# Performance work log

Measured on AMD Instinct MI355X. Metric: run time of the kernel, lower is better.

Reference implementation:

```python
import jax, jax.numpy as jnp
import numpy as np

W = 64          # word_embedding_size
ES = 64         # entity_embedding_size
H = 4           # head_num
DH = W // H
K = 3           # convolution_num
NW, NQ, NE, NR = 50000, 20000, 200000, 100000
LQ, LR, EP, B = 8, 16, 500000, 1024
D = ES + W      # propagated entity feature dim


def _mhsa_mean(x, Wq, bq, Wk, bk, Wv, bv, Wo, bo):
    # x: [N, L, W] -> [N, W]; standard multi-head self-attention then mean over L
    N, L, _ = x.shape
    q = (x @ Wq + bq).reshape(N, L, H, DH)
    k = (x @ Wk + bk).reshape(N, L, H, DH)
    v = (x @ Wv + bv).reshape(N, L, H, DH)
    s = jnp.einsum('nlhd,nmhd->nhlm', q, k) / jnp.sqrt(jnp.asarray(DH, x.dtype))
    a = jax.nn.softmax(s, axis=-1)
    o = jnp.einsum('nhlm,nmhd->nlhd', a, v).reshape(N, L, W)
    return (o @ Wo + bo).mean(axis=1)


def setup_inputs() -> dict:
    key = jax.random.key(0)
    ks = jax.random.split(key, 20)
    f = jnp.float32
    inp = {
        'word_emb': jax.random.normal(ks[0], (NW, W), f) * 0.02,
        'entity_emb': jax.random.normal(ks[1], (NE, ES), f) * 0.02,
        'Wq': jax.random.normal(ks[2], (W, W), f) * (1.0 / np.sqrt(W)),
        'bq': jnp.zeros((W,), f),
        'Wk': jax.random.normal(ks[3], (W, W), f) * (1.0 / np.sqrt(W)),
        'bk': jnp.zeros((W,), f),
        'Wv': jax.random.normal(ks[4], (W, W), f) * (1.0 / np.sqrt(W)),
        'bv': jnp.zeros((W,), f),
        'Wo': jax.random.normal(ks[5], (W, W), f) * (1.0 / np.sqrt(W)),
        'bo': jnp.zeros((W,), f),
        'review_words': jax.random.randint(ks[6], (NR, LR), 0, NW),
        'query_words_graph': jax.random.randint(ks[7], (NQ, LQ), 0, NW),
        'profile_dst': jax.random.randint(ks[8], (NR,), 0, NE),
        'pur_src': jax.random.randint(ks[9], (EP,), 0, NE),
        'pur_dst': jax.random.randint(ks[10], (EP,), 0, NE),
        'pur_qid': jax.random.randint(ks[11], (EP,), 0, NQ),
        'users': jax.random.randint(ks[12], (B,), 0, NE),
        'items': jax.random.randint(ks[13], (B,), 0, NE),
        'negs': jax.random.randint(ks[14], (B,), 0, NE),
        'query_words': jax.random.randint(ks[15], (B, LQ), 0, NW),
    }
    return inp


def reference(word_emb, entity_emb, Wq, bq, Wk, bk, Wv, bv, Wo, bo,
              review_words, query_words_graph, profile_dst,
              pur_src, pur_dst, pur_qid, users, items, negs, query_words):
    seg = jax.ops.segment_sum
    attn = lambda x: _mhsa_mean(x, Wq, bq, Wk, bk, Wv, bv, Wo, bo)
    we = word_emb.at[0].set(0.0)  # padding_idx=0

    # composes: word -> review / query (mailbox attention reduce)
    rev_h = attn(we[review_words])              # [NR, W]
    q_h = attn(we[query_words_graph])           # [NQ, W]
    q_e0 = jnp.concatenate([jnp.zeros((NQ, ES), we.dtype), q_h], axis=-1)  # [NQ, D]

    # profiles: review -> entity, mean by in-degree
    deg_p = jnp.clip(seg(jnp.ones((NR,), we.dtype), profile_dst, num_segments=NE), 1.0)[:, None]
    prof = seg(rev_h, profile_dst, num_segments=NE) / deg_p   # [NE, W]
    e = jnp.concatenate([entity_emb, prof], axis=-1)          # e_0: [NE, D]

    # deg_i = out_deg(purchased) + out_deg(purchased_by), clamped
    ones_e = jnp.ones((EP,), we.dtype)
    deg_i = jnp.clip(seg(ones_e, pur_src, num_segments=NE)
                     + seg(ones_e, pur_dst, num_segments=NE), 1.0)[:, None]
    inv = 1.0 / jnp.sqrt(deg_i)                               # [NE, 1]

    es = [e]
    for _ in range(K):
        msg = e * inv                                         # e_k / sqrt(deg_i)
        m_pur = e[pur_src] + q_e0[pur_qid] * inv[pur_src]     # msg_u_i UDF
        nxt = seg(m_pur, pur_dst, num_segments=NE) \
            + seg(msg[pur_dst], pur_src, num_segments=NE)     # purchased_by (reverse)
        e = nxt * inv
        es.append(e)
    efin = sum(es) / (K + 1)                                  # [NE, D]

    # batch scoring
    u = efin[users]
    qb = attn(we[query_words])                                # [B, W]
    p = u + jnp.concatenate([jnp.zeros((B, ES), we.dtype), qb], axis=-1)
    pos = jnp.sum(p * efin[items], axis=-1)
    neg = jnp.sum(p * efin[negs], axis=-1)
    loss = -jnp.mean(jax.nn.log_sigmoid(pos - neg))           # BPR loss
    return loss
```

## Files before the change

kernel.cpp:

```cpp
#include <hip/hip_runtime.h>
#include <hip/hip_fp8.h>
#include <cstdint>

#define CDIV(a,b) (((a)+(b)-1)/(b))

typedef __attribute__((ext_vector_type(8))) short bf16x8;
typedef __attribute__((ext_vector_type(4))) float f32x4;
typedef __attribute__((ext_vector_type(8))) float f32x8;
typedef __attribute__((ext_vector_type(4))) _Float16 half4;
typedef __attribute__((ext_vector_type(8))) _Float16 half8;

#define QK_SCALE 32.0f
#define SCORE_SCALE (0.25f / (QK_SCALE * QK_SCALE))
#define EXP2_C (SCORE_SCALE * 1.44269504089f)

#define ES_SCALE 64.0f

__device__ __forceinline__ float bf2f(short s) {
    return __builtin_bit_cast(float, ((unsigned)(unsigned short)s) << 16);
}
__device__ __forceinline__ short rtne(float f) {
    const unsigned u = __builtin_bit_cast(unsigned, f);
    return (short)((u + 0x7fffu + ((u >> 16) & 1u)) >> 16);
}
__device__ __forceinline__ unsigned pack2r(float lo, float hi) {
    return (unsigned)(unsigned short)rtne(lo) | ((unsigned)(unsigned short)rtne(hi) << 16);
}
__device__ __forceinline__ float fp8tof(unsigned char b) {
    __hip_fp8_e4m3 t; t.__x = b; return (float)t;
}
__device__ __forceinline__ unsigned char ftofp8(float f) {
    __hip_fp8_e4m3 t(f); return t.__x;
}
__device__ __forceinline__ f32x8 fp8x8tof32(long v) {
    union { long l; unsigned char b[8]; } u; u.l = v;
    f32x8 r;
    #pragma unroll
    for (int j = 0; j < 8; ++j) r[j] = fp8tof(u.b[j]);
    return r;
}
__device__ __forceinline__ long f32x8tofp8(f32x8 a) {
    union { long l; unsigned char b[8]; } u;
    #pragma unroll
    for (int j = 0; j < 8; ++j) u.b[j] = ftofp8(a[j]);
    return u.l;
}

template<int CTRL>
__device__ __forceinline__ float dpp_add(float x) {
    const int t = __builtin_amdgcn_update_dpp(0, __builtin_bit_cast(int, x),
                                              CTRL, 0xf, 0xf, true);
    return x + __builtin_bit_cast(float, t);
}
__device__ __forceinline__ float rowsum16(float x) {
    x = dpp_add<0x108>(x);
    x = dpp_add<0x104>(x);
    x = dpp_add<0x102>(x);
    x = dpp_add<0x101>(x);
    return x;
}


__device__ __forceinline__ void prep_body(int bid,
    const float* __restrict__ we, const short* __restrict__ Wt,
    const float* __restrict__ bq, const float* __restrict__ bk,
    const float* __restrict__ bv, unsigned char* __restrict__ WQKV, int NW)
{
    const int wave = threadIdx.x >> 6;
    const int lane = threadIdx.x & 63;
    const int quad = lane >> 4;
    const int lm   = lane & 15;
    const int ntiles = CDIV(NW, 16);

    bf16x8 bfr[3][4][2];
    #pragma unroll
    for (int p = 0; p < 3; ++p)
        #pragma unroll
        for (int nt = 0; nt < 4; ++nt)
            #pragma unroll
            for (int kh = 0; kh < 2; ++kh)
                bfr[p][nt][kh] = *(const bf16x8*)(Wt + ((p*64 + nt*16 + lm)*64) + kh*32 + quad*8);
    float bias[3][4];
    #pragma unroll
    for (int nt = 0; nt < 4; ++nt) {
        bias[0][nt] = bq[nt*16 + lm];
        bias[1][nt] = bk[nt*16 + lm];
        bias[2][nt] = bv[nt*16 + lm];
    }

    #pragma unroll
    for (int t = 0; t < 4; ++t) {
        const int tile = (bid*4 + wave)*4 + t;
        if (tile >= ntiles) return;
        const int wb = tile*16;
        int w = wb + lm;
        if (w >= NW) w = NW - 1;
        const float* xr = we + (size_t)w*64;
        union { unsigned u[4]; bf16x8 v; } a0, a1;
        const float4 f0 = *(const float4*)(xr + quad*8);
        const float4 f1 = *(const float4*)(xr + quad*8 + 4);
        const float4 f2 = *(const float4*)(xr + 32 + quad*8);
        const float4 f3 = *(const float4*)(xr + 32 + quad*8 + 4);
        a0.u[0] = pack2r(f0.x, f0.y); a0.u[1] = pack2r(f0.z, f0.w);
        a0.u[2] = pack2r(f1.x, f1.y); a0.u[3] = pack2r(f1.z, f1.w);
        a1.u[0] = pack2r(f2.x, f2.y); a1.u[1] = pack2r(f2.z, f2.w);
        a1.u[2] = pack2r(f3.x, f3.y); a1.u[3] = pack2r(f3.z, f3.w);
        if (w == 0) {
            a0.u[0]=0u; a0.u[1]=0u; a0.u[2]=0u; a0.u[3]=0u;
            a1.u[0]=0u; a1.u[1]=0u; a1.u[2]=0u; a1.u[3]=0u;
        }
        #pragma unroll
        for (int p = 0; p < 3; ++p) {
            #pragma unroll
            for (int nt = 0; nt < 4; ++nt) {
                f32x4 c = {bias[p][nt], bias[p][nt], bias[p][nt], bias[p][nt]};
                c = __builtin_amdgcn_mfma_f32_16x16x32_bf16(a0.v, bfr[p][nt][0], c, 0, 0, 0);
                c = __builtin_amdgcn_mfma_f32_16x16x32_bf16(a1.v, bfr[p][nt][1], c, 0, 0, 0);
                #pragma unroll
                for (int r = 0; r < 4; ++r) {
                    const int w2 = wb + quad*4 + r;
                    if (w2 < NW) {
                        unsigned char* rowo = WQKV + (size_t)w2*192;
                        const int base = (p == 2) ? 128 : (p == 0) ? 64 : 0;
                        rowo[base + nt*16 + lm] = ftofp8(c[r] * QK_SCALE);
                    }
                }
            }
        }
    }
}

__device__ __forceinline__ void fill_body(int bid,
    const int* __restrict__ src, const int* __restrict__ dst,
    const int* __restrict__ qid,
    int* __restrict__ curC, int2* __restrict__ cmb2, int EP)
{
    const int t = bid*256 + threadIdx.x;
    if (t >= EP) return;
    const int s = src[t], d = dst[t];
    const int p1 = atomicAdd(&curC[d], 1);
    int2 e1; e1.x = s; e1.y = qid[t];
    cmb2[p1] = e1;
    const int p2 = atomicAdd(&curC[s], 1);
    int2 e2; e2.x = d | (int)0x80000000; e2.y = 0;
    cmb2[p2] = e2;
}

__device__ __forceinline__ void expand_body(int bid, int nb, unsigned targ,
    const int* __restrict__ slist, const int* __restrict__ pn,
    const int* __restrict__ offC, const int* __restrict__ endC,
    const int2* __restrict__ cmb2, unsigned* __restrict__ lev,
    int* __restrict__ dl1, int* __restrict__ dn1,
    int* __restrict__ dl2, int* __restrict__ dn2)
{
    const int n = *pn;
    const int stride = nb * 256;
    for (int t = bid*256 + threadIdx.x; t < n; t += stride) {
        const int v = slist[t];
        const int b0 = offC[v], e0 = endC[v];
        for (int i = b0; i < e0; ++i) {
            const int u = cmb2[i].x & 0x7fffffff;
            const unsigned old = atomicMax(&lev[u], targ);
            if (old < targ) {
                dl1[atomicAdd(dn1, 1)] = u;
                if (dl2) dl2[atomicAdd(dn2, 1)] = u;
            }
        }
    }
}

__device__ __forceinline__ void finalize_body(int bid,
    const float* __restrict__ emb, const float* __restrict__ prof,
    unsigned char* __restrict__ e8, float* __restrict__ inv,
    const unsigned* __restrict__ deg_p, const unsigned* __restrict__ cntC, int NE)
{
    const int t = bid*256 + threadIdx.x;
    const int v = t >> 5;
    if (v >= NE) return;
    const int c = (t & 31) * 4;
    float4 ev;
    if (c < 64) {
        ev = *(const float4*)&emb[(size_t)v*64 + c];
    } else {
        ev = *(const float4*)&prof[(size_t)v*64 + (c - 64)];
        const unsigned dp = deg_p[v];
        const float r = 1.0f / (float)(dp > 1u ? dp : 1u);
        ev.x *= r; ev.y *= r; ev.z *= r; ev.w *= r;
    }
    union { unsigned u; unsigned char b[4]; } pk;
    pk.b[0] = ftofp8(ev.x * ES_SCALE);
    pk.b[1] = ftofp8(ev.y * ES_SCALE);
    pk.b[2] = ftofp8(ev.z * ES_SCALE);
    pk.b[3] = ftofp8(ev.w * ES_SCALE);
    *(unsigned*)&e8[(size_t)v*128 + c] = pk.u;
    if (c == 0) {
        const unsigned di = cntC[v];
        inv[v] = 1.0f / sqrtf((float)(di > 1u ? di : 1u));
    }
}

__device__ __forceinline__ void gather_body(int bid,
    const unsigned char* __restrict__ e8, const int* __restrict__ users,
    const int* __restrict__ items, const int* __restrict__ negs,
    float* __restrict__ acc, int B)
{
    const int t = bid*256 + threadIdx.x;
    const int r = t >> 4;
    if (r >= 3*B) return;
    const int c = (t & 15) * 8;
    const int which = r / B, b = r - which*B;
    const int idx = (which == 0) ? users[b] : (which == 1) ? items[b] : negs[b];
    const long ev = *(const long*)&e8[(size_t)idx*128 + c];
    f32x8 a = *(const f32x8*)&acc[(size_t)r*128 + c];
    a += fp8x8tof32(ev);
    *(f32x8*)&acc[(size_t)r*128 + c] = a;
}

__device__ __forceinline__ void prop1_body(int bid, int nb,
    const unsigned char* __restrict__ e_cur, const _Float16* __restrict__ q_h16,
    const float* __restrict__ inv,
    const int* __restrict__ offC, const int* __restrict__ endC,
    const int2* __restrict__ cmb2,
    const int* __restrict__ list, const int* __restrict__ pn,
    unsigned char* __restrict__ e_nxt, _Float16* __restrict__ qc)
{
    const int n = *pn;
    const int stride = nb * 256;
    for (int t = bid*256 + threadIdx.x; (t >> 4) < n; t += stride) {
        const int v = list[t >> 4];
        const int c = (t & 15) * 8;
        const bool qlane = (c >= 64);
        f32x8 a  = {0.f,0.f,0.f,0.f,0.f,0.f,0.f,0.f};
        f32x8 qa = {0.f,0.f,0.f,0.f,0.f,0.f,0.f,0.f};
        const int b0 = offC[v], e0 = endC[v];
        for (int i = b0; i < e0; ++i) {
            const int2 e = cmb2[i];
            const int u = e.x & 0x7fffffff;
            const float w = (e.x < 0) ? inv[u] : 1.0f;
            a += fp8x8tof32(*(const long*)&e_cur[(size_t)u*128 + c]) * w;
            if (e.x >= 0 && qlane) {
                const half8 qh = *(const half8*)&q_h16[(size_t)e.y*64 + (c - 64)];
                qa += __builtin_convertvector(qh, f32x8) * inv[u];
            }
        }
        if (qlane) {
            qa *= ES_SCALE;
            *(half8*)&qc[(size_t)v*64 + (c - 64)] = __builtin_convertvector(qa, half8);
            a += qa;
        }
        a *= inv[v];
        *(long*)&e_nxt[(size_t)v*128 + c] = f32x8tofp8(a);
    }
}

__device__ __forceinline__ void prop_list_body(int bid, int nb,
    const unsigned char* __restrict__ e_cur, const _Float16* __restrict__ qc,
    const float* __restrict__ inv,
    const int* __restrict__ offC, const int* __restrict__ endC,
    const int2* __restrict__ cmb2,
    const int* __restrict__ list, const int* __restrict__ pn,
    unsigned char* __restrict__ e_nxt)
{
    const int n = *pn;
    const int stride = nb * 256;
    for (int t = bid*256 + threadIdx.x; (t >> 4) < n; t += stride) {
        const int v = list[t >> 4];
        const int c = (t & 15) * 8;
        f32x8 a = {0.f,0.f,0.f,0.f,0.f,0.f,0.f,0.f};
        if (c >= 64) {
            const half8 q = *(const half8*)&qc[(size_t)v*64 + (c - 64)];
            a = __builtin_convertvector(q, f32x8);
        }
        const int b0 = offC[v], e0 = endC[v];
        int un = (b0 < e0) ? cmb2[b0].x : 0;
        for (int i = b0; i < e0; ++i) {
            const int uc = un;
            if (i + 1 < e0) un = cmb2[i + 1].x;
            const int u = uc & 0x7fffffff;
            const long es = *(const long*)&e_cur[(size_t)u*128 + c];
            const float w = (uc < 0) ? inv[u] : 1.0f;
            a += fp8x8tof32(es) * w;
        }
        a *= inv[v];
        *(long*)&e_nxt[(size_t)v*128 + c] = f32x8tofp8(a);
    }
}

struct TileRegs { int4 v0; long qf[4], kf[4]; };

__device__ __forceinline__ void load_tile(
    const unsigned char* __restrict__ WQKV, int w, int quad, TileRegs& t)
{
    const unsigned char* row = WQKV + (size_t)w * 192;
    t.v0 = *(const int4*)(row + 128 + quad*16);
    #pragma unroll
    for (int h = 0; h < 4; ++h) {
        if (quad < 2) {
            t.kf[h] = *(const long*)(row +      h*16 + quad*8);
            t.qf[h] = *(const long*)(row + 64 + h*16 + quad*8);
        } else {
            t.kf[h] = 0; t.qf[h] = 0;
        }
    }
}

template<int L, int MODE>
__device__ __forceinline__ void attn_body(
    unsigned char* __restrict__ smem,
    const unsigned char* __restrict__ WQKV, const int* __restrict__ words,
    const short* __restrict__ WoT, const float* __restrict__ bo,
    int N, void* __restrict__ outp, const int* __restrict__ sidx, int bid)
{
    constexpr int SPT = 16 / L;
    constexpr int SB  = 16 * SPT;
    unsigned char (*v_s)[16*80] = (unsigned char (*)[16*80])smem;
    float (*pbar_s)[64]         = (float (*)[64])(smem + 5120);
    float (*mo_s)[68]           = (float (*)[68])(smem + 6144);

    const int wave = threadIdx.x >> 6;
    const int lane = threadIdx.x & 63;
    const int quad = lane >> 4;
    const int lm   = lane & 15;
    const int tok_total = N * L;
    const float invL = 1.0f / ((float)L * QK_SCALE);

    int wid[4];
    #pragma unroll
    for (int t = 0; t < 4; ++t) {
        int tg = (bid*16 + wave*4 + t)*16 + lm;
        if (tg >= tok_total) tg = tok_total - 1;
        wid[t] = words[tg];
    }

    TileRegs cur, nxt;
    load_tile(WQKV, wid[0], quad, cur);

    #pragma unroll
    for (int ti = 0; ti < 4; ++ti) {
        if (ti < 3) load_tile(WQKV, wid[ti+1], quad, nxt);

        *(int4*)&v_s[wave][lm*80 + quad*16] = cur.v0;

        const bool mvalid = (SPT == 1) ? true : ((quad >> 1) == ((lm >> 3) & 1));

        #pragma unroll
        for (int h = 0; h < 4; ++h) {
            const f32x4 s4 = __builtin_amdgcn_mfma_f32_16x16x32_fp8_fp8(
                cur.kf[h], cur.qf[h], (f32x4){0.f,0.f,0.f,0.f}, 0, 0, 0);
            float sv0 = s4[0], sv1 = s4[1], sv2 = s4[2], sv3 = s4[3];
            if (!mvalid) { sv0 = sv1 = sv2 = sv3 = -3.0e38f; }
            float p0 = __builtin_amdgcn_exp2f(sv0*EXP2_C),
                  p1 = __builtin_amdgcn_exp2f(sv1*EXP2_C),
                  p2 = __builtin_amdgcn_exp2f(sv2*EXP2_C),
                  p3 = __builtin_amdgcn_exp2f(sv3*EXP2_C);
            float sm = p0+p1+p2+p3;
            sm += __shfl_xor(sm, 16, 64);
            sm += __shfl_xor(sm, 32, 64);
            const float rinv = __builtin_amdgcn_rcpf(sm);
            p0 *= rinv; p1 *= rinv; p2 *= rinv; p3 *= rinv;
            p0 = rowsum16(p0); p1 = rowsum16(p1);
            p2 = rowsum16(p2); p3 = rowsum16(p3);
            if (lm == 0) {
                pbar_s[wave][h*16 + quad*4 + 0] = p0 * invL;
                pbar_s[wave][h*16 + quad*4 + 1] = p1 * invL;
                pbar_s[wave][h*16 + quad*4 + 2] = p2 * invL;
                pbar_s[wave][h*16 + quad*4 + 3] = p3 * invL;
            }
        }

        #pragma unroll
        for (int s = 0; s < SPT; ++s) {
            f32x4 pb[4];
            #pragma unroll
            for (int j = 0; j < 4; ++j)
                pb[j] = *(const f32x4*)&pbar_s[wave][quad*16 + j*4];
            float o = 0.f;
            #pragma unroll
            for (int j2 = 0; j2 < L; ++j2) {
                const int m = s*L + j2;
                o += pb[m >> 2][m & 3] * fp8tof(v_s[wave][m*80 + lane]);
            }
            mo_s[(wave*4+ti)*SPT + s][lane] = o;
        }

        if (ti < 3) {
            cur.v0 = nxt.v0;
            #pragma unroll
            for (int h = 0; h < 4; ++h) { cur.qf[h] = nxt.qf[h]; cur.kf[h] = nxt.kf[h]; }
        }
    }
    __syncthreads();

    const int col = wave*16 + lm;
    const short* bT = WoT + col*64;
    const bf16x8 b0 = *(const bf16x8*)(bT + quad*8);
    const bf16x8 b1 = *(const bf16x8*)(bT + 32 + quad*8);
    const float boc = bo[col];
    #pragma unroll
    for (int rt = 0; rt < SPT; ++rt) {
        const float* ar = mo_s[rt*16 + lm];
        const float4 fA0 = *(const float4*)(ar + quad*8);
        const float4 fA1 = *(const float4*)(ar + quad*8 + 4);
        const float4 fA2 = *(const float4*)(ar + 32 + quad*8);
        const float4 fA3 = *(const float4*)(ar + 32 + quad*8 + 4);
        union { unsigned u[4]; bf16x8 v; } a0, a1;
        a0.u[0] = pack2r(fA0.x, fA0.y); a0.u[1] = pack2r(fA0.z, fA0.w);
        a0.u[2] = pack2r(fA1.x, fA1.y); a0.u[3] = pack2r(fA1.z, fA1.w);
        a1.u[0] = pack2r(fA2.x, fA2.y); a1.u[1] = pack2r(fA2.z, fA2.w);
        a1.u[2] = pack2r(fA3.x, fA3.y); a1.u[3] = pack2r(fA3.z, fA3.w);
        f32x4 c = {boc, boc, boc, boc};
        c = __builtin_amdgcn_mfma_f32_16x16x32_bf16(a0.v, b0, c, 0, 0, 0);
        c = __builtin_amdgcn_mfma_f32_16x16x32_bf16(a1.v, b1, c, 0, 0, 0);
        #pragma unroll
        for (int r = 0; r < 4; ++r) {
            const int seq = bid*SB + rt*16 + quad*4 + r;
            if (seq < N) {
                if (MODE == 0)
                    ((float*)outp)[(size_t)seq*64 + col] = c[r];
                else if (MODE == 1)
                    atomicAdd(&((float*)outp)[(size_t)sidx[seq]*64 + col], c[r]);
                else
                    ((_Float16*)outp)[(size_t)seq*64 + col] = (_Float16)c[r];
            }
        }
    }
}


__global__ __launch_bounds__(256) void misc_kernel(
    const int* __restrict__ src, const int* __restrict__ dst,
    unsigned* __restrict__ cntC, int EP,
    const int* __restrict__ pdst, unsigned* __restrict__ deg_p, int NR,
    const float* __restrict__ Wo, short* __restrict__ WoT,
    const float* __restrict__ Wq, const float* __restrict__ Wk,
    const float* __restrict__ Wv, short* __restrict__ Wt,
    const int* __restrict__ users, const int* __restrict__ items,
    const int* __restrict__ negs, int B, unsigned* __restrict__ lev,
    int* __restrict__ listS, int* __restrict__ list2, int* __restrict__ list1,
    int* __restrict__ nS, int* __restrict__ n2, int* __restrict__ n1,
    float4* __restrict__ prof_z, float4* __restrict__ acc_z,
    int prof4, int acc4, int nbM0)
{
    if ((int)blockIdx.x >= nbM0) {
        const int z = ((int)blockIdx.x - nbM0)*256 + (int)threadIdx.x;
        const float4 zero4 = {0.f, 0.f, 0.f, 0.f};
        if (z < prof4) prof_z[z] = zero4;
        else if (z - prof4 < acc4) acc_z[z - prof4] = zero4;
        return;
    }
    const int t = blockIdx.x*256 + threadIdx.x;
    if (t < EP) {
        const int s = src[t], d = dst[t];
        atomicAdd(&cntC[d], 1u); atomicAdd(&cntC[s], 1u);
    }
    if (t < NR) atomicAdd(&deg_p[pdst[t]], 1u);
    if (t < 4096) {
        const int j = t >> 6, k = t & 63;
        WoT[j*64 + k] = rtne(Wo[k*64 + j]);
    }
    if (t < 3*4096) {
        const int p = t >> 12, n = (t >> 6) & 63, k = t & 63;
        const float* W = (p==0) ? Wq : (p==1) ? Wk : Wv;
        Wt[t] = rtne(W[k*64 + n]);
    }
    if (t < 3*B) {
        const int which = t / B, b = t - which*B;
        const int v = (which == 0) ? users[b] : (which == 1) ? items[b] : negs[b];
        const unsigned old = atomicMax(&lev[v], 3u);
        if (old < 3u) {
            listS[atomicAdd(nS, 1)] = v;
            list2[atomicAdd(n2, 1)] = v;
            list1[atomicAdd(n1, 1)] = v;
        }
    }
}

#define SCAN_CHUNK 2048

__device__ __forceinline__ void scan_reduce_body(int b,
    const unsigned* __restrict__ cnt, unsigned* __restrict__ part, int n)
{
    const int base = b * SCAN_CHUNK;
    unsigned s = 0;
    #pragma unroll
    for (int i = 0; i < 8; ++i) {
        const int idx = base + i*256 + threadIdx.x;
        if (idx < n) s += cnt[idx];
    }
    #pragma unroll
    for (int off = 1; off < 64; off <<= 1) s += __shfl_xor(s, off, 64);
    __shared__ unsigned wsum[4];
    if ((threadIdx.x & 63) == 0) wsum[threadIdx.x >> 6] = s;
    __syncthreads();
    if (threadIdx.x == 0) part[b] = wsum[0]+wsum[1]+wsum[2]+wsum[3];
}

__global__ __launch_bounds__(256) void mega_scan_prep(
    const unsigned* __restrict__ cnt, unsigned* __restrict__ part, int n, int NB,
    const float* __restrict__ we, const short* __restrict__ Wt,
    const float* __restrict__ bq, const float* __restrict__ bk,
    const float* __restrict__ bv, unsigned char* __restrict__ WQKV, int NW)
{
    const int b = blockIdx.x;
    if (b < NB) scan_reduce_body(b, cnt, part, n);
    else        prep_body(b - NB, we, Wt, bq, bk, bv, WQKV, NW);
}

__global__ __launch_bounds__(1024) void scan_part_kernel(
    unsigned* __restrict__ part, int NB)
{
    __shared__ unsigned a[1024];
    const int t = threadIdx.x;
    a[t] = (t < NB) ? part[t] : 0u;
    __syncthreads();
    for (int d = 1; d < 1024; d <<= 1) {
        const unsigned xa = (t >= d) ? a[t-d] : 0u;
        __syncthreads();
        a[t] += xa;
        __syncthreads();
    }
    if (t < NB) part[t] = (t > 0) ? a[t-1] : 0u;
}

__global__ __launch_bounds__(256) void scan_final_kernel(
    const unsigned* __restrict__ cnt, const unsigned* __restrict__ part,
    int* __restrict__ off, int* __restrict__ cur, int n)
{
    const int b = blockIdx.x;
    __shared__ unsigned v[SCAN_CHUNK];
    __shared__ unsigned tsum[256];
    const int base = b * SCAN_CHUNK;
    const int t = threadIdx.x;
    #pragma unroll
    for (int i = 0; i < 8; ++i) {
        const int idx = base + i*256 + t;
        v[i*256 + t] = (idx < n) ? cnt[idx] : 0u;
    }
    __syncthreads();
    unsigned s = 0;
    #pragma unroll
    for (int i = 0; i < 8; ++i) s += v[t*8 + i];
    tsum[t] = s;
    __syncthreads();
    for (int d = 1; d < 256; d <<= 1) {
        const unsigned x = (t >= d) ? tsum[t-d] : 0u;
        __syncthreads();
        tsum[t] += x;
        __syncthreads();
    }
    unsigned run = ((t > 0) ? tsum[t-1] : 0u) + part[b];
    #pragma unroll
    for (int i = 0; i < 8; ++i) {
        const int idx = base + t*8 + i;
        if (idx < n) { off[idx] = (int)run; cur[idx] = (int)run; run += v[t*8+i]; }
    }
}

__global__ __launch_bounds__(256) void mega_attn(
    const unsigned char* __restrict__ WQKV,
    const int* __restrict__ src, const int* __restrict__ dst,
    const int* __restrict__ qid, int* __restrict__ curC,
    int2* __restrict__ cmb2, int EP, int nbF,
    const int* __restrict__ w1, int N1, float* __restrict__ o1,
    const int* __restrict__ sidx1, int nb1,
    const int* __restrict__ w2, int N2, _Float16* __restrict__ o2, int nb2,
    const int* __restrict__ w3, int N3, float* __restrict__ o3,
    const short* __restrict__ WoT, const float* __restrict__ bo)
{
    __shared__ __align__(16) unsigned char smem[6144 + 32*68*4];
    const int b = blockIdx.x;
    const int total = (int)gridDim.x;
    int W = (3*total)/5;
    if (W < nbF) W = nbF;
    const int wstart = total - W;
    int ba = b;
    if (b >= wstart) {
        const int local = b - wstart;
        const int f0 = (int)(((long)local * nbF) / W);
        const int f1 = (int)(((long)(local + 1) * nbF) / W);
        if (f1 > f0) {
            fill_body(f0, src, dst, qid, curC, cmb2, EP);
            return;
        }
        ba = b - f0;
    }
    if (ba < nb1)
        attn_body<16,1>(smem, WQKV, w1, WoT, bo, N1, o1, sidx1, ba);
    else if (ba < nb1 + nb2)
        attn_body<8,2>(smem, WQKV, w2, WoT, bo, N2, o2, nullptr, ba - nb1);
    else
        attn_body<8,0>(smem, WQKV, w3, WoT, bo, N3, o3, nullptr, ba - nb1 - nb2);
}

__global__ __launch_bounds__(256) void expand_kernel(
    unsigned targ, const int* __restrict__ slist, const int* __restrict__ pn,
    const int* __restrict__ offC, const int* __restrict__ endC,
    const int2* __restrict__ cmb2, unsigned* __restrict__ lev,
    int* __restrict__ dl1, int* __restrict__ dn1,
    int* __restrict__ dl2, int* __restrict__ dn2)
{
    expand_body(blockIdx.x, gridDim.x, targ, slist, pn, offC, endC, cmb2, lev,
                dl1, dn1, dl2, dn2);
}

__global__ __launch_bounds__(256) void mega_final(
    const int* __restrict__ list2, const int* __restrict__ n2,
    const int* __restrict__ offC, const int* __restrict__ endC,
    const int2* __restrict__ cmb2, unsigned* __restrict__ lev,
    int* __restrict__ list1, int* __restrict__ n1,
    const float* __restrict__ emb, const float* __restrict__ prof,
    unsigned char* __restrict__ e8, float* __restrict__ inv,
    const unsigned* __restrict__ deg_p, const unsigned* __restrict__ cntC, int NE)
{
    const int b = blockIdx.x;
    if (b < 256)
        expand_body(b, 256, 1u, list2, n2, offC, endC, cmb2, lev,
                    list1, n1, nullptr, nullptr);
    else
        finalize_body(b - 256, emb, prof, e8, inv, deg_p, cntC, NE);
}

__global__ __launch_bounds__(256) void mega_prop1(
    const unsigned char* __restrict__ e_cur, const _Float16* __restrict__ q_h16,
    const float* __restrict__ inv,
    const int* __restrict__ offC, const int* __restrict__ endC,
    const int2* __restrict__ cmb2,
    const int* __restrict__ list1, const int* __restrict__ n1,
    unsigned char* __restrict__ e_nxt, _Float16* __restrict__ qc,
    const int* __restrict__ users, const int* __restrict__ items,
    const int* __restrict__ negs, float* __restrict__ acc, int B)
{
    const int b = blockIdx.x;
    if (b < 2048) prop1_body(b, 2048, e_cur, q_h16, inv, offC, endC, cmb2,
                             list1, n1, e_nxt, qc);
    else          gather_body(b - 2048, e_cur, users, items, negs, acc, B);
}

__global__ __launch_bounds__(256) void mega_pg(
    const unsigned char* __restrict__ e_cur, const _Float16* __restrict__ qc,
    const float* __restrict__ inv,
    const int* __restrict__ offC, const int* __restrict__ endC,
    const int2* __restrict__ cmb2,
    const int* __restrict__ list2, const int* __restrict__ n2,
    unsigned char* __restrict__ e_nxt,
    const int* __restrict__ users, const int* __restrict__ items,
    const int* __restrict__ negs, float* __restrict__ acc, int B)
{
    const int b = blockIdx.x;
    if (b < 512) prop_list_body(b, 512, e_cur, qc, inv, offC, endC, cmb2,
                                list2, n2, e_nxt);
    else         gather_body(b - 512, e_cur, users, items, negs, acc, B);
}

__global__ __launch_bounds__(256) void prop_batch_kernel(
    const unsigned char* __restrict__ e_cur, const _Float16* __restrict__ qc,
    const float* __restrict__ inv,
    const int* __restrict__ offC, const int* __restrict__ endC,
    const int2* __restrict__ cmb2,
    const int* __restrict__ users, const int* __restrict__ items,
    const int* __restrict__ negs, float* __restrict__ acc, int B)
{
    const int t = blockIdx.x*256 + threadIdx.x;
    const int r = t >> 4;
    if (r >= 3*B) return;
    const int c = (t & 15) * 8;
    const int which = r / B, b = r - which*B;
    const int v = (which == 0) ? users[b] : (which == 1) ? items[b] : negs[b];
    f32x8 a = {0.f,0.f,0.f,0.f,0.f,0.f,0.f,0.f};
    if (c >= 64) {
        const half8 q = *(const half8*)&qc[(size_t)v*64 + (c - 64)];
        a = __builtin_convertvector(q, f32x8);
    }
    const int b0 = offC[v], e0 = endC[v];
    int un = (b0 < e0) ? cmb2[b0].x : 0;
    for (int i = b0; i < e0; ++i) {
        const int uc = un;
        if (i + 1 < e0) un = cmb2[i + 1].x;
        const int u = uc & 0x7fffffff;
        const long es = *(const long*)&e_cur[(size_t)u*128 + c];
        const float w = (uc < 0) ? inv[u] : 1.0f;
        a += fp8x8tof32(es) * w;
    }
    a *= inv[v];
    a += fp8x8tof32(*(const long*)&e_cur[(size_t)v*128 + c]);
    f32x8 ac = *(const f32x8*)&acc[(size_t)r*128 + c];
    ac += a;
    *(f32x8*)&acc[(size_t)r*128 + c] = ac;
}

__global__ __launch_bounds__(128) void loss_kernel(
    const float* __restrict__ acc, const float* __restrict__ qb,
    float* __restrict__ out, int B, float invB)
{
    const int b = blockIdx.x, d = threadIdx.x;
    const float u = acc[(size_t)b*128 + d] * (0.25f / ES_SCALE);
    const float p = u + (d >= 64 ? qb[(size_t)b*64 + (d - 64)] : 0.f);
    const float ei = acc[(size_t)(B + b)*128 + d];
    const float en = acc[(size_t)(2*B + b)*128 + d];
    float x = p * (ei - en) * (0.25f / ES_SCALE);
    #pragma unroll
    for (int off = 1; off < 64; off <<= 1) x += __shfl_xor(x, off, 64);
    __shared__ float wred[2];
    if ((threadIdx.x & 63) == 0) wred[threadIdx.x >> 6] = x;
    __syncthreads();
    if (threadIdx.x == 0) {
        const float xx = wred[0] + wred[1];
        const float ls = fminf(xx, 0.f) - log1pf(expf(-fabsf(xx)));
        atomicAdd(out, -ls * invB);
    }
}

extern "C" void kernel_launch(void* const* d_in, const int* in_sizes, int n_in,
                              void* d_out, int out_size, void* d_ws, size_t ws_size,
                              hipStream_t stream)
{
    const float* word_emb        = (const float*)d_in[0];
    const float* entity_emb      = (const float*)d_in[1];
    const float* Wq = (const float*)d_in[2];  const float* bq = (const float*)d_in[3];
    const float* Wk = (const float*)d_in[4];  const float* bk = (const float*)d_in[5];
    const float* Wv = (const float*)d_in[6];  const float* bv = (const float*)d_in[7];
    const float* Wo = (const float*)d_in[8];  const float* bo = (const float*)d_in[9];
    const int* review_words      = (const int*)d_in[10];
    const int* query_words_graph = (const int*)d_in[11];
    const int* profile_dst       = (const int*)d_in[12];
    const int* pur_src           = (const int*)d_in[13];
    const int* pur_dst           = (const int*)d_in[14];
    const int* pur_qid           = (const int*)d_in[15];
    const int* users             = (const int*)d_in[16];
    const int* items             = (const int*)d_in[17];
    const int* negs              = (const int*)d_in[18];
    const int* query_words       = (const int*)d_in[19];

    const int NW = in_sizes[0]  / 64;
    const int NE = in_sizes[1]  / 64;
    const int NR = in_sizes[10] / 16;
    const int NQ = in_sizes[11] / 8;
    const int EP = in_sizes[13];
    const int B  = in_sizes[16];
    const int NB = CDIV(NE, SCAN_CHUNK);

    char* ws = (char*)d_ws;
    size_t off = 0;
    auto alloc = [&](size_t bytes) -> char* {
        char* q = ws + off; off += (bytes + 255) & ~(size_t)255; return q;
    };
    float*         prof  = (float*)         alloc((size_t)NE*64*4);
    unsigned char* e8A   = (unsigned char*) alloc((size_t)NE*128);
    unsigned char* e8B   = (unsigned char*) alloc((size_t)NE*128);
    _Float16*      q_h16 = (_Float16*)      alloc((size_t)NQ*64*2);
    float*         qb    = (float*)         alloc((size_t)B*64*4);
    float*         acc   = (float*)         alloc((size_t)3*B*128*4);
    unsigned*  deg_p   = (unsigned*) alloc((size_t)NE*4);
    unsigned*  cntC    = (unsigned*) alloc((size_t)NE*4);
    unsigned*  lev     = (unsigned*) alloc((size_t)NE*4);
    int*       fcnt    = (int*)      alloc(256);
    int*       offC    = (int*)      alloc((size_t)NE*4);
    int*       curC    = (int*)      alloc((size_t)NE*4);
    int2*      cmb2    = (int2*)     alloc((size_t)2*EP*8);
    int*       listS   = (int*)      alloc((size_t)3*B*4);
    int*       list2   = (int*)      alloc((size_t)NE*4);
    int*       list1   = (int*)      alloc((size_t)NE*4);
    float*     inv     = (float*)    alloc((size_t)NE*4);
    unsigned*  part    = (unsigned*) alloc((size_t)NB*4);
    short*     WoT     = (short*)    alloc((size_t)64*64*2);
    short*     Wt      = (short*)    alloc((size_t)3*64*64*2);

    if (off > ws_size) return;

    unsigned char* WQKV = e8A;
    _Float16* qc = (_Float16*)prof;
    int* nS = fcnt; int* n2 = fcnt + 1; int* n1 = fcnt + 2;

    const size_t zlen = (size_t)((char*)fcnt - (char*)deg_p) + 256;
    hipMemsetAsync(deg_p, 0, zlen, stream);
    hipMemsetAsync(d_out, 0, (size_t)out_size*4, stream);

    const int nbM0  = CDIV(EP, 256);
    const int prof4 = NE*16;
    const int acc4  = 3*B*32;
    const int nbZ   = CDIV(prof4 + acc4, 256);
    misc_kernel<<<nbM0 + nbZ, 256, 0, stream>>>(pur_src, pur_dst, cntC, EP,
        profile_dst, deg_p, NR, Wo, WoT, Wq, Wk, Wv, Wt,
        users, items, negs, B, lev, listS, list2, list1, nS, n2, n1,
        (float4*)prof, (float4*)acc, prof4, acc4, nbM0);

    const int nbP = CDIV(CDIV(NW, 16), 16);
    mega_scan_prep<<<NB + nbP, 256, 0, stream>>>(cntC, part, NE, NB,
        word_emb, Wt, bq, bk, bv, WQKV, NW);
    scan_part_kernel<<<1, 1024, 0, stream>>>(part, NB);
    scan_final_kernel<<<NB, 256, 0, stream>>>(cntC, part, offC, curC, NE);

    const int nbF = CDIV(EP, 256);
    const int nb1 = CDIV(NR, 16), nb2 = CDIV(NQ, 32), nb3 = CDIV(B, 32);
    mega_attn<<<nb1 + nb2 + nb3 + nbF, 256, 0, stream>>>(WQKV,
        pur_src, pur_dst, pur_qid, curC, cmb2, EP, nbF,
        review_words, NR, prof, profile_dst, nb1,
        query_words_graph, NQ, q_h16, nb2,
        query_words, B, qb, WoT, bo);

    expand_kernel<<<64, 256, 0, stream>>>(2u, listS, nS, offC, curC, cmb2, lev,
        list2, n2, list1, n1);

    mega_final<<<256 + CDIV(NE*32, 256), 256, 0, stream>>>(
        list2, n2, offC, curC, cmb2, lev, list1, n1,
        entity_emb, prof, e8A, inv, deg_p, cntC, NE);

    mega_prop1<<<2048 + CDIV(3*B*16, 256), 256, 0, stream>>>(
        e8A, q_h16, inv, offC, curC, cmb2, list1, n1, e8B, qc,
        users, items, negs, acc, B);

    mega_pg<<<512 + CDIV(3*B*16, 256), 256, 0, stream>>>(
        e8B, qc, inv, offC, curC, cmb2, list2, n2, e8A,
        users, items, negs, acc, B);

    prop_batch_kernel<<<CDIV(3*B*16, 256), 256, 0, stream>>>(e8A, qc, inv,
        offC, curC, cmb2, users, items, negs, acc, B);

    loss_kernel<<<B, 128, 0, stream>>>(acc, qb, (float*)d_out, B, 1.0f / (float)B);
}
```

Measured before the change: 457.0 us.

## Replace CSR frontier expansion with edge-parallel BFS fused into earlier kernels

The frontier expansion used to walk CSR adjacency from a seed list. It now scans the raw edge list in parallel, checking both endpoints' levels. This removes the need for the CSR to exist, so level-2 expansion moves into the scan/prep kernel and level-1 expansion into the attention/fill kernel. Two standalone launches (expand_kernel and the expansion half of mega_final) go away. The cost is reading all EP edges twice instead of only the frontier's neighbours. Correctness also now depends on level-2 expansion finishing before level-1 expansion begins, which kernel ordering provides.

New measurement: 800.2 us. +75.1%, slower.

```diff
diff --git a/kernel.cpp b/kernel.cpp
--- a/kernel.cpp
+++ b/kernel.cpp
@@ -146,24 +146,28 @@
     cmb2[p2] = e2;
 }
 
-__device__ __forceinline__ void expand_body(int bid, int nb, unsigned targ,
-    const int* __restrict__ slist, const int* __restrict__ pn,
-    const int* __restrict__ offC, const int* __restrict__ endC,
-    const int2* __restrict__ cmb2, unsigned* __restrict__ lev,
+__device__ __forceinline__ void eexp_body(int bid, int nb, unsigned targ,
+    const int* __restrict__ src, const int* __restrict__ dst, int EP,
+    unsigned* __restrict__ lev,
     int* __restrict__ dl1, int* __restrict__ dn1,
     int* __restrict__ dl2, int* __restrict__ dn2)
 {
-    const int n = *pn;
     const int stride = nb * 256;
-    for (int t = bid*256 + threadIdx.x; t < n; t += stride) {
-        const int v = slist[t];
-        const int b0 = offC[v], e0 = endC[v];
-        for (int i = b0; i < e0; ++i) {
-            const int u = cmb2[i].x & 0x7fffffff;
-            const unsigned old = atomicMax(&lev[u], targ);
+    for (int t = bid*256 + threadIdx.x; t < EP; t += stride) {
+        const int s = src[t], d = dst[t];
+        const unsigned ls = lev[s], ld = lev[d];
+        if (ls > targ && ld < targ) {
+            const unsigned old = atomicMax(&lev[d], targ);
             if (old < targ) {
-                dl1[atomicAdd(dn1, 1)] = u;
-                if (dl2) dl2[atomicAdd(dn2, 1)] = u;
+                dl1[atomicAdd(dn1, 1)] = d;
+                if (dl2) dl2[atomicAdd(dn2, 1)] = d;
+            }
+        }
+        if (ld > targ && ls < targ) {
+            const unsigned old = atomicMax(&lev[s], targ);
+            if (old < targ) {
+                dl1[atomicAdd(dn1, 1)] = s;
+                if (dl2) dl2[atomicAdd(dn2, 1)] = s;
             }
         }
     }
@@ -499,11 +503,17 @@
     const unsigned* __restrict__ cnt, unsigned* __restrict__ part, int n, int NB,
     const float* __restrict__ we, const short* __restrict__ Wt,
     const float* __restrict__ bq, const float* __restrict__ bk,
-    const float* __restrict__ bv, unsigned char* __restrict__ WQKV, int NW)
+    const float* __restrict__ bv, unsigned char* __restrict__ WQKV, int NW, int nbP,
+    const int* __restrict__ src, const int* __restrict__ dst, int EP,
+    unsigned* __restrict__ lev,
+    int* __restrict__ list2, int* __restrict__ n2,
+    int* __restrict__ list1, int* __restrict__ n1)
 {
     const int b = blockIdx.x;
-    if (b < NB) scan_reduce_body(b, cnt, part, n);
-    else        prep_body(b - NB, we, Wt, bq, bk, bv, WQKV, NW);
+    if (b < NB)            scan_reduce_body(b, cnt, part, n);
+    else if (b < NB + nbP) prep_body(b - NB, we, Wt, bq, bk, bv, WQKV, NW);
+    else                   eexp_body(b - NB - nbP, 256, 2u, src, dst, EP, lev,
+                                     list2, n2, list1, n1);
 }
 
 __global__ __launch_bounds__(1024) void scan_part_kernel(
@@ -561,6 +571,7 @@
     const int* __restrict__ src, const int* __restrict__ dst,
     const int* __restrict__ qid, int* __restrict__ curC,
     int2* __restrict__ cmb2, int EP, int nbF,
+    unsigned* __restrict__ lev, int* __restrict__ list1, int* __restrict__ n1,
     const int* __restrict__ w1, int N1, float* __restrict__ o1,
     const int* __restrict__ sidx1, int nb1,
     const int* __restrict__ w2, int N2, _Float16* __restrict__ o2, int nb2,
@@ -570,16 +581,21 @@
     __shared__ __align__(16) unsigned char smem[6144 + 32*68*4];
     const int b = blockIdx.x;
     const int total = (int)gridDim.x;
+    const int nbS = nbF + 128;
     int W = (3*total)/5;
-    if (W < nbF) W = nbF;
+    if (W < nbS) W = nbS;
     const int wstart = total - W;
     int ba = b;
     if (b >= wstart) {
         const int local = b - wstart;
-        const int f0 = (int)(((long)local * nbF) / W);
-        const int f1 = (int)(((long)(local + 1) * nbF) / W);
+        const int f0 = (int)(((long)local * nbS) / W);
+        const int f1 = (int)(((long)(local + 1) * nbS) / W);
         if (f1 > f0) {
-            fill_body(f0, src, dst, qid, curC, cmb2, EP);
+            if (f0 < nbF)
+                fill_body(f0, src, dst, qid, curC, cmb2, EP);
+            else
+                eexp_body(f0 - nbF, 128, 1u, src, dst, EP, lev,
+                          list1, n1, nullptr, nullptr);
             return;
         }
         ba = b - f0;
@@ -592,32 +608,12 @@
         attn_body<8,0>(smem, WQKV, w3, WoT, bo, N3, o3, nullptr, ba - nb1 - nb2);
 }
 
-__global__ __launch_bounds__(256) void expand_kernel(
-    unsigned targ, const int* __restrict__ slist, const int* __restrict__ pn,
-    const int* __restrict__ offC, const int* __restrict__ endC,
-    const int2* __restrict__ cmb2, unsigned* __restrict__ lev,
-    int* __restrict__ dl1, int* __restrict__ dn1,
-    int* __restrict__ dl2, int* __restrict__ dn2)
-{
-    expand_body(blockIdx.x, gridDim.x, targ, slist, pn, offC, endC, cmb2, lev,
-                dl1, dn1, dl2, dn2);
-}
-
-__global__ __launch_bounds__(256) void mega_final(
-    const int* __restrict__ list2, const int* __restrict__ n2,
-    const int* __restrict__ offC, const int* __restrict__ endC,
-    const int2* __restrict__ cmb2, unsigned* __restrict__ lev,
-    int* __restrict__ list1, int* __restrict__ n1,
+__global__ __launch_bounds__(256) void finalize_kernel(
     const float* __restrict__ emb, const float* __restrict__ prof,
     unsigned char* __restrict__ e8, float* __restrict__ inv,
     const unsigned* __restrict__ deg_p, const unsigned* __restrict__ cntC, int NE)
 {
-    const int b = blockIdx.x;
-    if (b < 256)
-        expand_body(b, 256, 1u, list2, n2, offC, endC, cmb2, lev,
-                    list1, n1, nullptr, nullptr);
-    else
-        finalize_body(b - 256, emb, prof, e8, inv, deg_p, cntC, NE);
+    finalize_body(blockIdx.x, emb, prof, e8, inv, deg_p, cntC, NE);
 }
 
 __global__ __launch_bounds__(256) void mega_prop1(
@@ -785,24 +781,22 @@
         (float4*)prof, (float4*)acc, prof4, acc4, nbM0);
 
     const int nbP = CDIV(CDIV(NW, 16), 16);
-    mega_scan_prep<<<NB + nbP, 256, 0, stream>>>(cntC, part, NE, NB,
-        word_emb, Wt, bq, bk, bv, WQKV, NW);
+    mega_scan_prep<<<NB + nbP + 256, 256, 0, stream>>>(cntC, part, NE, NB,
+        word_emb, Wt, bq, bk, bv, WQKV, NW, nbP,
+        pur_src, pur_dst, EP, lev, list2, n2, list1, n1);
     scan_part_kernel<<<1, 1024, 0, stream>>>(part, NB);
     scan_final_kernel<<<NB, 256, 0, stream>>>(cntC, part, offC, curC, NE);
 
     const int nbF = CDIV(EP, 256);
     const int nb1 = CDIV(NR, 16), nb2 = CDIV(NQ, 32), nb3 = CDIV(B, 32);
-    mega_attn<<<nb1 + nb2 + nb3 + nbF, 256, 0, stream>>>(WQKV,
+    mega_attn<<<nb1 + nb2 + nb3 + nbF + 128, 256, 0, stream>>>(WQKV,
         pur_src, pur_dst, pur_qid, curC, cmb2, EP, nbF,
+        lev, list1, n1,
         review_words, NR, prof, profile_dst, nb1,
         query_words_graph, NQ, q_h16, nb2,
         query_words, B, qb, WoT, bo);
 
-    expand_kernel<<<64, 256, 0, stream>>>(2u, listS, nS, offC, curC, cmb2, lev,
-        list2, n2, list1, n1);
-
-    mega_final<<<256 + CDIV(NE*32, 256), 256, 0, stream>>>(
-        list2, n2, offC, curC, cmb2, lev, list1, n1,
+    finalize_kernel<<<CDIV(NE*32, 256), 256, 0, stream>>>(
         entity_emb, prof, e8A, inv, deg_p, cntC, NE);
 
     mega_prop1<<<2048 + CDIV(3*B*16, 256), 256, 0, stream>>>(
```

## Record per-edge ranks during counting and fold partial scan into final scan

Applied to the files above, without the earlier changes.

The degree-counting atomics now store their returned old value as a per-edge rank, so CSR fill computes slots as offset plus rank instead of doing a second round of atomics. The separate single-block partial-sum scan kernel is removed; each final-scan block sums the preceding block partials itself with wave reductions, and the end-pointer array is written directly as offset plus count. This removes one kernel launch and the fill atomics, at the cost of two extra EP-sized int arrays written and read, plus a small redundant prefix sum in every scan block.

Result: faster. 436.9 us (-4.4%).

```diff
diff --git a/kernel.cpp b/kernel.cpp
--- a/kernel.cpp
+++ b/kernel.cpp
@@ -133,15 +133,17 @@
 __device__ __forceinline__ void fill_body(int bid,
     const int* __restrict__ src, const int* __restrict__ dst,
     const int* __restrict__ qid,
-    int* __restrict__ curC, int2* __restrict__ cmb2, int EP)
+    const int* __restrict__ offC,
+    const int* __restrict__ rankD, const int* __restrict__ rankS,
+    int2* __restrict__ cmb2, int EP)
 {
     const int t = bid*256 + threadIdx.x;
     if (t >= EP) return;
     const int s = src[t], d = dst[t];
-    const int p1 = atomicAdd(&curC[d], 1);
+    const int p1 = offC[d] + rankD[t];
     int2 e1; e1.x = s; e1.y = qid[t];
     cmb2[p1] = e1;
-    const int p2 = atomicAdd(&curC[s], 1);
+    const int p2 = offC[s] + rankS[t];
     int2 e2; e2.x = d | (int)0x80000000; e2.y = 0;
     cmb2[p2] = e2;
 }
@@ -429,7 +431,8 @@
 
 __global__ __launch_bounds__(256) void misc_kernel(
     const int* __restrict__ src, const int* __restrict__ dst,
-    unsigned* __restrict__ cntC, int EP,
+    unsigned* __restrict__ cntC, int* __restrict__ rankD, int* __restrict__ rankS,
+    int EP,
     const int* __restrict__ pdst, unsigned* __restrict__ deg_p, int NR,
     const float* __restrict__ Wo, short* __restrict__ WoT,
     const float* __restrict__ Wq, const float* __restrict__ Wk,
@@ -451,7 +454,8 @@
     const int t = blockIdx.x*256 + threadIdx.x;
     if (t < EP) {
         const int s = src[t], d = dst[t];
-        atomicAdd(&cntC[d], 1u); atomicAdd(&cntC[s], 1u);
+        rankD[t] = (int)atomicAdd(&cntC[d], 1u);
+        rankS[t] = (int)atomicAdd(&cntC[s], 1u);
     }
     if (t < NR) atomicAdd(&deg_p[pdst[t]], 1u);
     if (t < 4096) {
@@ -506,22 +510,6 @@
     else        prep_body(b - NB, we, Wt, bq, bk, bv, WQKV, NW);
 }
 
-__global__ __launch_bounds__(1024) void scan_part_kernel(
-    unsigned* __restrict__ part, int NB)
-{
-    __shared__ unsigned a[1024];
-    const int t = threadIdx.x;
-    a[t] = (t < NB) ? part[t] : 0u;
-    __syncthreads();
-    for (int d = 1; d < 1024; d <<= 1) {
-        const unsigned xa = (t >= d) ? a[t-d] : 0u;
-        __syncthreads();
-        a[t] += xa;
-        __syncthreads();
-    }
-    if (t < NB) part[t] = (t > 0) ? a[t-1] : 0u;
-}
-
 __global__ __launch_bounds__(256) void scan_final_kernel(
     const unsigned* __restrict__ cnt, const unsigned* __restrict__ part,
     int* __restrict__ off, int* __restrict__ cur, int n)
@@ -529,14 +517,20 @@
     const int b = blockIdx.x;
     __shared__ unsigned v[SCAN_CHUNK];
     __shared__ unsigned tsum[256];
+    __shared__ unsigned wsum2[4];
     const int base = b * SCAN_CHUNK;
     const int t = threadIdx.x;
+    unsigned pv = (t < b) ? part[t] : 0u;
+    #pragma unroll
+    for (int o = 1; o < 64; o <<= 1) pv += __shfl_xor(pv, o, 64);
+    if ((t & 63) == 0) wsum2[t >> 6] = pv;
     #pragma unroll
     for (int i = 0; i < 8; ++i) {
         const int idx = base + i*256 + t;
         v[i*256 + t] = (idx < n) ? cnt[idx] : 0u;
     }
     __syncthreads();
+    const unsigned pbase = wsum2[0]+wsum2[1]+wsum2[2]+wsum2[3];
     unsigned s = 0;
     #pragma unroll
     for (int i = 0; i < 8; ++i) s += v[t*8 + i];
@@ -548,18 +542,24 @@
         tsum[t] += x;
         __syncthreads();
     }
-    unsigned run = ((t > 0) ? tsum[t-1] : 0u) + part[b];
+    unsigned run = ((t > 0) ? tsum[t-1] : 0u) + pbase;
     #pragma unroll
     for (int i = 0; i < 8; ++i) {
         const int idx = base + t*8 + i;
-        if (idx < n) { off[idx] = (int)run; cur[idx] = (int)run; run += v[t*8+i]; }
+        if (idx < n) {
+            const unsigned c = v[t*8+i];
+            off[idx] = (int)run;
+            cur[idx] = (int)(run + c);
+            run += c;
+        }
     }
 }
 
 __global__ __launch_bounds__(256) void mega_attn(
     const unsigned char* __restrict__ WQKV,
     const int* __restrict__ src, const int* __restrict__ dst,
-    const int* __restrict__ qid, int* __restrict__ curC,
+    const int* __restrict__ qid, const int* __restrict__ offC,
+    const int* __restrict__ rankD, const int* __restrict__ rankS,
     int2* __restrict__ cmb2, int EP, int nbF,
     const int* __restrict__ w1, int N1, float* __restrict__ o1,
     const int* __restrict__ sidx1, int nb1,
@@ -579,7 +579,7 @@
         const int f0 = (int)(((long)local * nbF) / W);
         const int f1 = (int)(((long)(local + 1) * nbF) / W);
         if (f1 > f0) {
-            fill_body(f0, src, dst, qid, curC, cmb2, EP);
+            fill_body(f0, src, dst, qid, offC, rankD, rankS, cmb2, EP);
             return;
         }
         ba = b - f0;
@@ -757,6 +757,8 @@
     int*       offC    = (int*)      alloc((size_t)NE*4);
     int*       curC    = (int*)      alloc((size_t)NE*4);
     int2*      cmb2    = (int2*)     alloc((size_t)2*EP*8);
+    int*       rankD   = (int*)      alloc((size_t)EP*4);
+    int*       rankS   = (int*)      alloc((size_t)EP*4);
     int*       listS   = (int*)      alloc((size_t)3*B*4);
     int*       list2   = (int*)      alloc((size_t)NE*4);
     int*       list1   = (int*)      alloc((size_t)NE*4);
@@ -779,7 +781,8 @@
     const int prof4 = NE*16;
     const int acc4  = 3*B*32;
     const int nbZ   = CDIV(prof4 + acc4, 256);
-    misc_kernel<<<nbM0 + nbZ, 256, 0, stream>>>(pur_src, pur_dst, cntC, EP,
+    misc_kernel<<<nbM0 + nbZ, 256, 0, stream>>>(pur_src, pur_dst, cntC,
+        rankD, rankS, EP,
         profile_dst, deg_p, NR, Wo, WoT, Wq, Wk, Wv, Wt,
         users, items, negs, B, lev, listS, list2, list1, nS, n2, n1,
         (float4*)prof, (float4*)acc, prof4, acc4, nbM0);
@@ -787,13 +790,12 @@
     const int nbP = CDIV(CDIV(NW, 16), 16);
     mega_scan_prep<<<NB + nbP, 256, 0, stream>>>(cntC, part, NE, NB,
         word_emb, Wt, bq, bk, bv, WQKV, NW);
-    scan_part_kernel<<<1, 1024, 0, stream>>>(part, NB);
     scan_final_kernel<<<NB, 256, 0, stream>>>(cntC, part, offC, curC, NE);
 
     const int nbF = CDIV(EP, 256);
     const int nb1 = CDIV(NR, 16), nb2 = CDIV(NQ, 32), nb3 = CDIV(B, 32);
     mega_attn<<<nb1 + nb2 + nb3 + nbF, 256, 0, stream>>>(WQKV,
-        pur_src, pur_dst, pur_qid, curC, cmb2, EP, nbF,
+        pur_src, pur_dst, pur_qid, offC, rankD, rankS, cmb2, EP, nbF,
         review_words, NR, prof, profile_dst, nb1,
         query_words_graph, NQ, q_h16, nb2,
         query_words, B, qb, WoT, bo);
```
